# Kernel tuning notes

Hardware: AMD Instinct MI355X
Metric: run time of the kernel (lower is better)

Reference implementation:

```python
import jax, jax.numpy as jnp
import numpy as np

EMBED_DIM = 1024
NUM_HEADS = 16
NUM_KV_HEADS = 4
HEAD_DIM = 64
WINDOW_SIZE = 32
TOKENS_PER_FRAME = 64
BASE_T, BASE_D, BASE_B = 10000.0, 100.0, 100.0


def apply_3d_rope(x, pos_t, pos_d, pos_b):
    # x: (B, S, H, D); pos_*: (S,) int
    D = x.shape[-1]
    half = D // 2
    dim_idx = jnp.arange(half, dtype=jnp.float32)
    inv_freq = 1.0 / (BASE_T ** (2.0 * dim_idx / D))  # (half,)
    ang = (pos_t.astype(jnp.float32)[:, None] * inv_freq
           + pos_d.astype(jnp.float32)[:, None] * inv_freq * (BASE_T / BASE_D)
           + pos_b.astype(jnp.float32)[:, None] * inv_freq * (BASE_T / BASE_B))  # (S, half)
    cos = jnp.cos(ang)[None, :, None, :]
    sin = jnp.sin(ang)[None, :, None, :]
    x1 = x[..., 0::2]
    x2 = x[..., 1::2]
    y1 = x1 * cos - x2 * sin
    y2 = x1 * sin + x2 * cos
    return jnp.stack([y1, y2], axis=-1).reshape(x.shape)


def setup_inputs() -> dict:
    key = jax.random.key(0)
    ks = jax.random.split(key, 8)
    B, Sn, Lp = 1, 1024, 4096
    hidden_states = jax.random.normal(ks[0], (B, Sn, EMBED_DIM), dtype=jnp.float32)
    past_k = jax.random.normal(ks[1], (B, NUM_KV_HEADS, Lp, HEAD_DIM), dtype=jnp.float32)
    past_v = jax.random.normal(ks[2], (B, NUM_KV_HEADS, Lp, HEAD_DIM), dtype=jnp.float32)
    wq = jax.random.normal(ks[3], (EMBED_DIM, NUM_HEADS * HEAD_DIM), dtype=jnp.float32) * 0.02
    wk = jax.random.normal(ks[4], (EMBED_DIM, NUM_KV_HEADS * HEAD_DIM), dtype=jnp.float32) * 0.02
    wv = jax.random.normal(ks[5], (EMBED_DIM, NUM_KV_HEADS * HEAD_DIM), dtype=jnp.float32) * 0.02
    wo = jax.random.normal(ks[6], (NUM_HEADS * HEAD_DIM, EMBED_DIM), dtype=jnp.float32) * 0.02
    # frame-time positions: tokens_per_frame tokens share a frame time; past frames 0..63, new frames 64..79
    past_idx = jnp.arange(Lp, dtype=jnp.int32)
    new_idx = jnp.arange(Sn, dtype=jnp.int32)
    past_t = past_idx // TOKENS_PER_FRAME
    new_t = new_idx // TOKENS_PER_FRAME + Lp // TOKENS_PER_FRAME
    # 8x8 depth-by-bearing patch grid within each frame
    past_d = (past_idx % TOKENS_PER_FRAME) // 8
    past_b = past_idx % 8
    new_d = (new_idx % TOKENS_PER_FRAME) // 8
    new_b = new_idx % 8
    return dict(hidden_states=hidden_states, past_k=past_k, past_v=past_v,
                wq=wq, wk=wk, wv=wv, wo=wo,
                new_t=new_t, new_d=new_d, new_b=new_b,
                past_t=past_t, past_d=past_d, past_b=past_b)


def reference(hidden_states, past_k, past_v, wq, wk, wv, wo,
              new_t, new_d, new_b, past_t, past_d, past_b):
    B, Sn, _ = hidden_states.shape
    Lp = past_t.shape[0]
    Q = (hidden_states @ wq).reshape(B, Sn, NUM_HEADS, HEAD_DIM)
    Kn = (hidden_states @ wk).reshape(B, Sn, NUM_KV_HEADS, HEAD_DIM)
    Vn = (hidden_states @ wv).reshape(B, Sn, NUM_KV_HEADS, HEAD_DIM)
    Q = apply_3d_rope(Q, new_t, new_d, new_b)
    Kn = apply_3d_rope(Kn, new_t, new_d, new_b)
    Q = Q.transpose(0, 2, 1, 3)   # (B, H, Sn, D)
    Kn = Kn.transpose(0, 2, 1, 3)  # (B, KVH, Sn, D)
    Vn = Vn.transpose(0, 2, 1, 3)
    # Sliding-window truncation on frame time: torch does searchsorted + slice
    # (drop past keys with time < min_time). Masking those keys to -inf is
    # mathematically identical and jit-friendly (static shapes).
    min_time = new_t.max() - (WINDOW_SIZE - 1)
    past_keep = past_t >= min_time                                    # (Lp,)
    valid = jnp.concatenate([past_keep, jnp.ones((Sn,), dtype=bool)])  # (Lp+Sn,)
    pos_t = jnp.concatenate([past_t, new_t])
    K = jnp.concatenate([past_k, Kn], axis=2)  # (B, KVH, Lp+Sn, D)
    V = jnp.concatenate([past_v, Vn], axis=2)
    rep = NUM_HEADS // NUM_KV_HEADS
    K = jnp.repeat(K, rep, axis=1)  # (B, H, L, D) -- repeat_interleave semantics
    V = jnp.repeat(V, rep, axis=1)
    scores = jnp.einsum('bhqd,bhkd->bhqk', Q, K) / jnp.sqrt(jnp.float32(HEAD_DIM))
    mask = (pos_t[None, :] <= new_t[:, None]) & valid[None, :]  # (Sn, L) frame-causal + window
    scores = jnp.where(mask[None, None], scores, jnp.float32(-jnp.inf))
    attn = jax.nn.softmax(scores, axis=-1)
    attn = jnp.nan_to_num(attn)  # fully-masked rows -> 0 (matches torch nan_to_num)
    out = jnp.einsum('bhqk,bhkd->bhqd', attn, V)
    out = out.transpose(0, 2, 1, 3).reshape(B, Sn, NUM_HEADS * HEAD_DIM)
    out = out @ wo
    return out, Kn, Vn
```

## Files before the change

### kernel.cpp

```cpp
#include <hip/hip_runtime.h>
#include <math.h>

#define EMBED 1024
#define NH 16
#define NKV 4
#define HD 64
#define SN 1024
#define LP 4096
#define WIN 32

#define FREQ_C 0.4152410118609203f

typedef float floatx4 __attribute__((ext_vector_type(4)));
typedef __bf16 bf16x8 __attribute__((ext_vector_type(8)));

__global__ __launch_bounds__(256) void qkv_mfma_kernel(
    const float* __restrict__ hidden, const float* __restrict__ wq,
    const float* __restrict__ wk, const float* __restrict__ wv,
    const int* __restrict__ new_t, const int* __restrict__ new_d,
    const int* __restrict__ new_b,
    float* __restrict__ qws, float* __restrict__ knp, float* __restrict__ vnp)
{
    __shared__ __bf16 ASh[64][72];
    __shared__ __bf16 BSh[64][72];

    const int tid = threadIdx.x;
    const int lane = tid & 63, w = tid >> 6;
    const int g = lane >> 4, c = lane & 15;
    const int bx = blockIdx.x, by = blockIdx.y;

    int mode, ldb, cbase;
    const float* W;
    if (bx < 16)      { mode = 0; W = wq; ldb = 1024; cbase = bx * 64; }
    else if (bx < 20) { mode = 1; W = wk; ldb = 256;  cbase = (bx - 16) * 64; }
    else              { mode = 2; W = wv; ldb = 256;  cbase = (bx - 20) * 64; }

    const int arow = tid >> 2, ak = (tid & 3) * 16;
    const float* Ap = hidden + (size_t)(by * 64 + arow) * EMBED + ak;
    const int bn = tid & 63, bk0 = (tid >> 6) * 16;
    const float* Bp = W + (size_t)bk0 * ldb + cbase + bn;

    floatx4 acc[4] = {floatx4(0.f), floatx4(0.f), floatx4(0.f), floatx4(0.f)};

    float a0[16], b0[16];
#pragma unroll
    for (int i = 0; i < 4; i++)
        *(float4*)&a0[4 * i] = *(const float4*)(Ap + 4 * i);
#pragma unroll
    for (int j = 0; j < 16; j++) b0[j] = Bp[(size_t)j * ldb];

    const int strip = w * 16;

    for (int k0 = 0; k0 < EMBED; k0 += 64) {
        __syncthreads();
        {
            bf16x8 av0, av1, bv0, bv1;
#pragma unroll
            for (int j = 0; j < 8; j++) {
                av0[j] = (__bf16)a0[j];     av1[j] = (__bf16)a0[j + 8];
                bv0[j] = (__bf16)b0[j];     bv1[j] = (__bf16)b0[j + 8];
            }
            *(bf16x8*)&ASh[arow][ak] = av0;
            *(bf16x8*)&ASh[arow][ak + 8] = av1;
            *(bf16x8*)&BSh[bn][bk0] = bv0;
            *(bf16x8*)&BSh[bn][bk0 + 8] = bv1;
        }
        __syncthreads();
        if (k0 + 64 < EMBED) {
#pragma unroll
            for (int i = 0; i < 4; i++)
                *(float4*)&a0[4 * i] = *(const float4*)(Ap + k0 + 64 + 4 * i);
#pragma unroll
            for (int j = 0; j < 16; j++) b0[j] = Bp[(size_t)(k0 + 64 + j) * ldb];
        }
        bf16x8 af0 = *(const bf16x8*)&ASh[strip + c][g * 8];
        bf16x8 af1 = *(const bf16x8*)&ASh[strip + c][32 + g * 8];
#pragma unroll
        for (int t = 0; t < 4; t++) {
            bf16x8 bf0 = *(const bf16x8*)&BSh[t * 16 + c][g * 8];
            bf16x8 bf1 = *(const bf16x8*)&BSh[t * 16 + c][32 + g * 8];
            acc[t] = __builtin_amdgcn_mfma_f32_16x16x32_bf16(af0, bf0, acc[t], 0, 0, 0);
            acc[t] = __builtin_amdgcn_mfma_f32_16x16x32_bf16(af1, bf1, acc[t], 0, 0, 0);
        }
    }

    const int m0 = strip + g * 4;
    if (mode == 2) {
        const int kvh = bx - 20;
#pragma unroll
        for (int r = 0; r < 4; r++) {
            const int token = by * 64 + m0 + r;
#pragma unroll
            for (int t = 0; t < 4; t++)
                vnp[((size_t)kvh * SN + token) * HD + t * 16 + c] = acc[t][r];
        }
    } else {
        float fr[4];
#pragma unroll
        for (int t = 0; t < 4; t++) {
            const int d = (cbase + t * 16 + c) & 63;
            fr[t] = exp2f(-FREQ_C * (float)(d >> 1));
        }
        const int par = c & 1;
#pragma unroll
        for (int r = 0; r < 4; r++) {
            const int token = by * 64 + m0 + r;
            const float ft = (float)new_t[token];
            const float fdb = (float)(new_d[token] + new_b[token]);
#pragma unroll
            for (int t = 0; t < 4; t++) {
                const float ang = ft * fr[t] + fdb * (fr[t] * 100.0f);
                float sv, cv;
                sincosf(ang, &sv, &cv);
                const float x = acc[t][r];
                const float xp = __shfl_xor(x, 1, 64);
                const float y = par ? (xp * sv + x * cv) : (x * cv - xp * sv);
                if (mode == 0) {
                    qws[(size_t)token * EMBED + cbase + t * 16 + c] = y;
                } else {
                    const int kvh = bx - 16;
                    knp[((size_t)kvh * SN + token) * HD + t * 16 + c] = y;
                }
            }
        }
    }
}

__global__ __launch_bounds__(256) void out_mfma_kernel(
    const float* __restrict__ A, const float* __restrict__ W,
    float* __restrict__ C)
{
    __shared__ __bf16 ASh[64][72];
    __shared__ __bf16 BSh[64][72];

    const int tid = threadIdx.x;
    const int lane = tid & 63, w = tid >> 6;
    const int g = lane >> 4, c = lane & 15;
    const int bx = blockIdx.x, by = blockIdx.y;

    const int arow = tid >> 2, ak = (tid & 3) * 16;
    const float* Ap = A + (size_t)(by * 64 + arow) * EMBED + ak;
    const int bn = tid & 63, bk0 = (tid >> 6) * 16;
    const float* Bp = W + (size_t)bk0 * EMBED + bx * 64 + bn;

    floatx4 acc[4] = {floatx4(0.f), floatx4(0.f), floatx4(0.f), floatx4(0.f)};

    float a0[16], b0[16];
#pragma unroll
    for (int i = 0; i < 4; i++)
        *(float4*)&a0[4 * i] = *(const float4*)(Ap + 4 * i);
#pragma unroll
    for (int j = 0; j < 16; j++) b0[j] = Bp[(size_t)j * EMBED];

    const int strip = w * 16;

    for (int k0 = 0; k0 < EMBED; k0 += 64) {
        __syncthreads();
        {
            bf16x8 av0, av1, bv0, bv1;
#pragma unroll
            for (int j = 0; j < 8; j++) {
                av0[j] = (__bf16)a0[j];     av1[j] = (__bf16)a0[j + 8];
                bv0[j] = (__bf16)b0[j];     bv1[j] = (__bf16)b0[j + 8];
            }
            *(bf16x8*)&ASh[arow][ak] = av0;
            *(bf16x8*)&ASh[arow][ak + 8] = av1;
            *(bf16x8*)&BSh[bn][bk0] = bv0;
            *(bf16x8*)&BSh[bn][bk0 + 8] = bv1;
        }
        __syncthreads();
        if (k0 + 64 < EMBED) {
#pragma unroll
            for (int i = 0; i < 4; i++)
                *(float4*)&a0[4 * i] = *(const float4*)(Ap + k0 + 64 + 4 * i);
#pragma unroll
            for (int j = 0; j < 16; j++) b0[j] = Bp[(size_t)(k0 + 64 + j) * EMBED];
        }
        bf16x8 af0 = *(const bf16x8*)&ASh[strip + c][g * 8];
        bf16x8 af1 = *(const bf16x8*)&ASh[strip + c][32 + g * 8];
#pragma unroll
        for (int t = 0; t < 4; t++) {
            bf16x8 bf0 = *(const bf16x8*)&BSh[t * 16 + c][g * 8];
            bf16x8 bf1 = *(const bf16x8*)&BSh[t * 16 + c][32 + g * 8];
            acc[t] = __builtin_amdgcn_mfma_f32_16x16x32_bf16(af0, bf0, acc[t], 0, 0, 0);
            acc[t] = __builtin_amdgcn_mfma_f32_16x16x32_bf16(af1, bf1, acc[t], 0, 0, 0);
        }
    }

    const int m0 = strip + g * 4;
#pragma unroll
    for (int r = 0; r < 4; r++) {
        const int row = by * 64 + m0 + r;
#pragma unroll
        for (int t = 0; t < 4; t++)
            C[(size_t)row * EMBED + bx * 64 + t * 16 + c] = acc[t][r];
    }
}

#define PREFETCH_CHUNK(CI)                                                     \
    {                                                                          \
        const int base_ = (myStart + (CI)) << 6;                               \
        const int gk_ = base_ + skk;                                           \
        if (gk_ < Nk) {                                                        \
            const float* kp_ = (gk_ < nPast)                                   \
                ? past_k + ((size_t)(kvh * LP + p0 + gk_)) * HD + sd0          \
                : knp + ((size_t)(kvh * SN + (gk_ - nPast))) * HD + sd0;       \
            kb0 = *(const float4*)(kp_ + 0);                                   \
            kb1 = *(const float4*)(kp_ + 4);                                   \
            kb2 = *(const float4*)(kp_ + 8);                                   \
            kb3 = *(const float4*)(kp_ + 12);                                  \
        } else {                                                               \
            kb0 = kb1 = kb2 = kb3 = make_float4(0.f, 0.f, 0.f, 0.f);           \
        }                                                                      \
        const int gv0_ = base_ + 2 * kp2;                                      \
        if (gv0_ < Nk) {                                                       \
            const float* vp_ = (gv0_ < nPast)                                  \
                ? past_v + ((size_t)(kvh * LP + p0 + gv0_)) * HD + vdb         \
                : vnp + ((size_t)(kvh * SN + (gv0_ - nPast))) * HD + vdb;      \
            vb00 = *(const float4*)(vp_ + 0);                                  \
            vb01 = *(const float4*)(vp_ + 4);                                  \
        } else {                                                               \
            vb00 = vb01 = make_float4(0.f, 0.f, 0.f, 0.f);                     \
        }                                                                      \
        const int gv1_ = gv0_ + 1;                                             \
        if (gv1_ < Nk) {                                                       \
            const float* vp_ = (gv1_ < nPast)                                  \
                ? past_v + ((size_t)(kvh * LP + p0 + gv1_)) * HD + vdb         \
                : vnp + ((size_t)(kvh * SN + (gv1_ - nPast))) * HD + vdb;      \
            vb10 = *(const float4*)(vp_ + 0);                                  \
            vb11 = *(const float4*)(vp_ + 4);                                  \
        } else {                                                               \
            vb10 = vb11 = make_float4(0.f, 0.f, 0.f, 0.f);                     \
        }                                                                      \
        if (tid < 64) {                                                        \
            const int g2_ = base_ + tid;                                       \
            ptreg = (g2_ < Nk)                                                 \
                ? ((g2_ < nPast) ? past_t[p0 + g2_] : new_t[g2_ - nPast])      \
                : 0x7fffffff;                                                  \
        }                                                                      \
    }

__global__ __launch_bounds__(256) void attn_kernel(
    const float* __restrict__ qws, const float* __restrict__ past_k,
    const float* __restrict__ past_v, const float* __restrict__ knp,
    const float* __restrict__ vnp, const int* __restrict__ new_t,
    const int* __restrict__ past_t, float* __restrict__ opart,
    float* __restrict__ lpart)
{
    __shared__ __bf16 KS[64][72];
    __shared__ __bf16 VS[64][72];
    __shared__ __bf16 PS[64][72];
    __shared__ float MSK[64];

    const int tid = threadIdx.x;
    const int f = blockIdx.x, h = blockIdx.y, sidx = blockIdx.z;
    const int kvh = h >> 2;
    const int lane = tid & 63, w = tid >> 6;
    const int g = lane >> 4, c = lane & 15;

    const int tmax = new_t[SN - 1];
    const int min_time = tmax - (WIN - 1);
    const int qtf = new_t[f * 64];

    int lo = 0, hi = LP;
    while (lo < hi) {
        int mid = (lo + hi) >> 1;
        if (past_t[mid] >= min_time) hi = mid; else lo = mid + 1;
    }
    const int p0 = lo;
    const int nPast = LP - p0;
    const int Nk = nPast + (f + 1) * 64;

    const int nch = (Nk + 63) >> 6;
    const int qch = nch >> 2, rem = nch & 3;
    const int myCount = qch + (sidx < rem ? 1 : 0);
    const int myStart = sidx * qch + (sidx < rem ? sidx : rem);

    bf16x8 aQ[2];
    {
        const int q = f * 64 + w * 16 + c;
        const float* qp = qws + (size_t)q * EMBED + h * HD + g * 8;
#pragma unroll
        for (int s = 0; s < 2; s++) {
            float4 q0 = *(const float4*)(qp + s * 32);
            float4 q1 = *(const float4*)(qp + s * 32 + 4);
            bf16x8 a;
            a[0] = (__bf16)q0.x; a[1] = (__bf16)q0.y;
            a[2] = (__bf16)q0.z; a[3] = (__bf16)q0.w;
            a[4] = (__bf16)q1.x; a[5] = (__bf16)q1.y;
            a[6] = (__bf16)q1.z; a[7] = (__bf16)q1.w;
            aQ[s] = a;
        }
    }

    floatx4 oacc[4] = {floatx4(0.f), floatx4(0.f), floatx4(0.f), floatx4(0.f)};
    floatx4 lacc = floatx4(0.f);
    bf16x8 bOnes;
#pragma unroll
    for (int j = 0; j < 8; j++) bOnes[j] = (__bf16)1.0f;

    const float scale = 0.125f;

    const int skk = tid >> 2, sd0 = (tid & 3) * 16;
    const int kp2 = tid & 31, vdb = (tid >> 5) * 8;

    float4 kb0, kb1, kb2, kb3;
    float4 vb00, vb01, vb10, vb11;
    int ptreg = 0x7fffffff;

    if (myCount > 0) PREFETCH_CHUNK(0);

    for (int chi = 0; chi < myCount; ++chi) {
        __syncthreads();

        {
            bf16x8 t0, t1;
            t0[0] = (__bf16)kb0.x; t0[1] = (__bf16)kb0.y;
            t0[2] = (__bf16)kb0.z; t0[3] = (__bf16)kb0.w;
            t0[4] = (__bf16)kb1.x; t0[5] = (__bf16)kb1.y;
            t0[6] = (__bf16)kb1.z; t0[7] = (__bf16)kb1.w;
            t1[0] = (__bf16)kb2.x; t1[1] = (__bf16)kb2.y;
            t1[2] = (__bf16)kb2.z; t1[3] = (__bf16)kb2.w;
            t1[4] = (__bf16)kb3.x; t1[5] = (__bf16)kb3.y;
            t1[6] = (__bf16)kb3.z; t1[7] = (__bf16)kb3.w;
            *(bf16x8*)&KS[skk][sd0] = t0;
            *(bf16x8*)&KS[skk][sd0 + 8] = t1;
        }
        {
            float e0[8] = {vb00.x, vb00.y, vb00.z, vb00.w,
                           vb01.x, vb01.y, vb01.z, vb01.w};
            float e1[8] = {vb10.x, vb10.y, vb10.z, vb10.w,
                           vb11.x, vb11.y, vb11.z, vb11.w};
#pragma unroll
            for (int j = 0; j < 8; j++) {
                union { __bf16 b[2]; unsigned u; } pk;
                pk.b[0] = (__bf16)e0[j];
                pk.b[1] = (__bf16)e1[j];
                *(unsigned*)&VS[vdb + j][2 * kp2] = pk.u;
            }
        }
        if (tid < 64) {
            const int g2 = ((myStart + chi) << 6) + tid;
            const bool ok = (ptreg <= qtf) && ((g2 >= nPast) || (ptreg >= min_time));
            MSK[tid] = ok ? 0.f : -1e30f;
        }
        __syncthreads();

        if (chi + 1 < myCount) PREFETCH_CHUNK(chi + 1);

        floatx4 sacc[4];
#pragma unroll
        for (int t = 0; t < 4; t++) {
            sacc[t] = floatx4(0.f);
#pragma unroll
            for (int s = 0; s < 2; s++) {
                bf16x8 b = *(const bf16x8*)&KS[t * 16 + c][s * 32 + g * 8];
                sacc[t] = __builtin_amdgcn_mfma_f32_16x16x32_bf16(aQ[s], b, sacc[t], 0, 0, 0);
            }
        }

#pragma unroll
        for (int r = 0; r < 4; r++)
#pragma unroll
            for (int t = 0; t < 4; t++)
                PS[w * 16 + g * 4 + r][t * 16 + c] =
                    (__bf16)__expf(sacc[t][r] * scale + MSK[t * 16 + c]);

#pragma unroll
        for (int s = 0; s < 2; s++) {
            bf16x8 a = *(const bf16x8*)&PS[w * 16 + c][s * 32 + g * 8];
            lacc = __builtin_amdgcn_mfma_f32_16x16x32_bf16(a, bOnes, lacc, 0, 0, 0);
#pragma unroll
            for (int t = 0; t < 4; t++) {
                bf16x8 b = *(const bf16x8*)&VS[t * 16 + c][s * 32 + g * 8];
                oacc[t] = __builtin_amdgcn_mfma_f32_16x16x32_bf16(a, b, oacc[t], 0, 0, 0);
            }
        }
    }

    float* Op = opart + ((size_t)(f * 16 + h) * 4 + sidx) * 4096;
    float* lp = lpart + ((size_t)(f * 16 + h) * 4 + sidx) * 64;
#pragma unroll
    for (int r = 0; r < 4; r++) {
        const int q = w * 16 + g * 4 + r;
#pragma unroll
        for (int t = 0; t < 4; t++)
            Op[(size_t)q * 64 + t * 16 + c] = oacc[t][r];
        if (c == 0) lp[q] = lacc[r];
    }
}

__global__ __launch_bounds__(256) void attn_merge_kernel(
    const float* __restrict__ opart, const float* __restrict__ lpart,
    float* __restrict__ ctx)
{
    const int f = blockIdx.x, h = blockIdx.y;
    const int tid = threadIdx.x;
    const int q = tid >> 2, d0 = (tid & 3) * 16;
    const size_t fh = (size_t)(f * 16 + h);

    float l = 0.f;
#pragma unroll
    for (int s = 0; s < 4; s++) l += lpart[(fh * 4 + s) * 64 + q];
    const float inv = (l > 0.f) ? (1.f / l) : 0.f;

    float o[16] = {};
#pragma unroll
    for (int s = 0; s < 4; s++) {
        const float* Os = opart + (fh * 4 + s) * 4096 + (size_t)q * 64 + d0;
#pragma unroll
        for (int v = 0; v < 4; v++) {
            float4 ov = *(const float4*)(Os + v * 4);
            o[v * 4 + 0] += ov.x;
            o[v * 4 + 1] += ov.y;
            o[v * 4 + 2] += ov.z;
            o[v * 4 + 3] += ov.w;
        }
    }
    float* cp = ctx + (size_t)(f * 64 + q) * EMBED + h * HD + d0;
#pragma unroll
    for (int v = 0; v < 4; v++)
        *(float4*)(cp + v * 4) = make_float4(o[v * 4] * inv, o[v * 4 + 1] * inv,
                                             o[v * 4 + 2] * inv, o[v * 4 + 3] * inv);
}

extern "C" void kernel_launch(void* const* d_in, const int* in_sizes, int n_in,
                              void* d_out, int out_size, void* d_ws, size_t ws_size,
                              hipStream_t stream) {
    const float* hidden = (const float*)d_in[0];
    const float* past_k = (const float*)d_in[1];
    const float* past_v = (const float*)d_in[2];
    const float* wq     = (const float*)d_in[3];
    const float* wk     = (const float*)d_in[4];
    const float* wv     = (const float*)d_in[5];
    const float* wo     = (const float*)d_in[6];
    const int* new_t    = (const int*)d_in[7];
    const int* new_d    = (const int*)d_in[8];
    const int* new_b    = (const int*)d_in[9];
    const int* past_t   = (const int*)d_in[10];

    float* out = (float*)d_out;
    float* knp = out + SN * EMBED;
    float* vnp = knp + NKV * SN * HD;

    float* qws   = (float*)d_ws;
    float* lpart = qws + (size_t)SN * EMBED;
    float* opart = lpart + (size_t)16 * 16 * 4 * 64;
    float* ctx   = opart + (size_t)16 * 16 * 4 * 4096;

    qkv_mfma_kernel<<<dim3(24, 16), 256, 0, stream>>>(
        hidden, wq, wk, wv, new_t, new_d, new_b, qws, knp, vnp);
    attn_kernel<<<dim3(16, 16, 4), 256, 0, stream>>>(
        qws, past_k, past_v, knp, vnp, new_t, past_t, opart, lpart);
    attn_merge_kernel<<<dim3(16, 16), 256, 0, stream>>>(opart, lpart, ctx);
    out_mfma_kernel<<<dim3(16, 16), 256, 0, stream>>>(ctx, wo, out);
}
```

Baseline: 156.8 us.

## Pre-convert inputs and weights to transposed bf16 and remap attention grid per XCD

Adds a prep kernel that converts hidden states to bf16 and transposes and converts wq/wk/wv/wo to bf16 so the GEMM kernels load contiguous 16-byte bf16 vectors instead of strided fp32 scalars. The merge kernel writes its context in bf16 to halve traffic into the output projection. The attention grid is flattened and remapped so blocks sharing a KV head are dispatched to the same XCD, aiming for better L2 reuse of past K/V. In exchange it adds an extra launch and re-converts the weights on every call.

```diff
diff --git a/kernel.cpp b/kernel.cpp
--- a/kernel.cpp
+++ b/kernel.cpp
@@ -14,9 +14,71 @@
 typedef float floatx4 __attribute__((ext_vector_type(4)));
 typedef __bf16 bf16x8 __attribute__((ext_vector_type(8)));
 
-__global__ __launch_bounds__(256) void qkv_mfma_kernel(
+__global__ __launch_bounds__(256) void prep_kernel(
     const float* __restrict__ hidden, const float* __restrict__ wq,
     const float* __restrict__ wk, const float* __restrict__ wv,
+    const float* __restrict__ wo,
+    __bf16* __restrict__ hidb, __bf16* __restrict__ wqT,
+    __bf16* __restrict__ wkT, __bf16* __restrict__ wvT,
+    __bf16* __restrict__ woT)
+{
+    const int jb = blockIdx.x, tid = threadIdx.x;
+    if (jb >= 640) {
+        const size_t base = (size_t)(jb - 640) * 4096 + (size_t)tid * 16;
+        float4 f0 = *(const float4*)(hidden + base);
+        float4 f1 = *(const float4*)(hidden + base + 4);
+        float4 f2 = *(const float4*)(hidden + base + 8);
+        float4 f3 = *(const float4*)(hidden + base + 12);
+        bf16x8 o0, o1;
+        o0[0] = (__bf16)f0.x; o0[1] = (__bf16)f0.y;
+        o0[2] = (__bf16)f0.z; o0[3] = (__bf16)f0.w;
+        o0[4] = (__bf16)f1.x; o0[5] = (__bf16)f1.y;
+        o0[6] = (__bf16)f1.z; o0[7] = (__bf16)f1.w;
+        o1[0] = (__bf16)f2.x; o1[1] = (__bf16)f2.y;
+        o1[2] = (__bf16)f2.z; o1[3] = (__bf16)f2.w;
+        o1[4] = (__bf16)f3.x; o1[5] = (__bf16)f3.y;
+        o1[6] = (__bf16)f3.z; o1[7] = (__bf16)f3.w;
+        *(bf16x8*)(hidb + base) = o0;
+        *(bf16x8*)(hidb + base + 8) = o1;
+        return;
+    }
+    const float* src; __bf16* dst; int N, tk, tn;
+    if (jb < 256)      { src = wq; dst = wqT; N = 1024; tk = jb >> 4;         tn = jb & 15; }
+    else if (jb < 320) { src = wk; dst = wkT; N = 256;  tk = (jb - 256) >> 2; tn = (jb - 256) & 3; }
+    else if (jb < 384) { src = wv; dst = wvT; N = 256;  tk = (jb - 320) >> 2; tn = (jb - 320) & 3; }
+    else               { src = wo; dst = woT; N = 1024; tk = (jb - 384) >> 4; tn = (jb - 384) & 15; }
+
+    __shared__ float T[64][65];
+    {
+        const int r = tid >> 2, c0 = (tid & 3) * 16;
+        const float* sp = src + (size_t)(tk * 64 + r) * N + tn * 64 + c0;
+        float4 v0 = *(const float4*)(sp + 0);
+        float4 v1 = *(const float4*)(sp + 4);
+        float4 v2 = *(const float4*)(sp + 8);
+        float4 v3 = *(const float4*)(sp + 12);
+        *(float4*)&T[r][c0 + 0] = v0;
+        *(float4*)&T[r][c0 + 4] = v1;
+        *(float4*)&T[r][c0 + 8] = v2;
+        *(float4*)&T[r][c0 + 12] = v3;
+    }
+    __syncthreads();
+    {
+        const int n = tid >> 2, k0 = (tid & 3) * 16;
+        bf16x8 o0, o1;
+#pragma unroll
+        for (int j = 0; j < 8; j++) {
+            o0[j] = (__bf16)T[k0 + j][n];
+            o1[j] = (__bf16)T[k0 + 8 + j][n];
+        }
+        __bf16* dp = dst + (size_t)(tn * 64 + n) * 1024 + tk * 64 + k0;
+        *(bf16x8*)dp = o0;
+        *(bf16x8*)(dp + 8) = o1;
+    }
+}
+
+__global__ __launch_bounds__(256) void qkv_mfma_kernel(
+    const __bf16* __restrict__ hidb, const __bf16* __restrict__ wqT,
+    const __bf16* __restrict__ wkT, const __bf16* __restrict__ wvT,
     const int* __restrict__ new_t, const int* __restrict__ new_d,
     const int* __restrict__ new_b,
     float* __restrict__ qws, float* __restrict__ knp, float* __restrict__ vnp)
@@ -29,49 +91,38 @@
     const int g = lane >> 4, c = lane & 15;
     const int bx = blockIdx.x, by = blockIdx.y;
 
-    int mode, ldb, cbase;
-    const float* W;
-    if (bx < 16)      { mode = 0; W = wq; ldb = 1024; cbase = bx * 64; }
-    else if (bx < 20) { mode = 1; W = wk; ldb = 256;  cbase = (bx - 16) * 64; }
-    else              { mode = 2; W = wv; ldb = 256;  cbase = (bx - 20) * 64; }
+    int mode, cbase;
+    const __bf16* W;
+    if (bx < 16)      { mode = 0; W = wqT; cbase = bx * 64; }
+    else if (bx < 20) { mode = 1; W = wkT; cbase = (bx - 16) * 64; }
+    else              { mode = 2; W = wvT; cbase = (bx - 20) * 64; }
 
     const int arow = tid >> 2, ak = (tid & 3) * 16;
-    const float* Ap = hidden + (size_t)(by * 64 + arow) * EMBED + ak;
+    const __bf16* Ap = hidb + (size_t)(by * 64 + arow) * EMBED + ak;
     const int bn = tid & 63, bk0 = (tid >> 6) * 16;
-    const float* Bp = W + (size_t)bk0 * ldb + cbase + bn;
+    const __bf16* Bp = W + (size_t)(cbase + bn) * 1024 + bk0;
 
     floatx4 acc[4] = {floatx4(0.f), floatx4(0.f), floatx4(0.f), floatx4(0.f)};
 
-    float a0[16], b0[16];
-#pragma unroll
-    for (int i = 0; i < 4; i++)
-        *(float4*)&a0[4 * i] = *(const float4*)(Ap + 4 * i);
-#pragma unroll
-    for (int j = 0; j < 16; j++) b0[j] = Bp[(size_t)j * ldb];
+    bf16x8 a0 = *(const bf16x8*)(Ap);
+    bf16x8 a1 = *(const bf16x8*)(Ap + 8);
+    bf16x8 b0 = *(const bf16x8*)(Bp);
+    bf16x8 b1 = *(const bf16x8*)(Bp + 8);
 
     const int strip = w * 16;
 
     for (int k0 = 0; k0 < EMBED; k0 += 64) {
         __syncthreads();
-        {
-            bf16x8 av0, av1, bv0, bv1;
-#pragma unroll
-            for (int j = 0; j < 8; j++) {
-                av0[j] = (__bf16)a0[j];     av1[j] = (__bf16)a0[j + 8];
-                bv0[j] = (__bf16)b0[j];     bv1[j] = (__bf16)b0[j + 8];
-            }
-            *(bf16x8*)&ASh[arow][ak] = av0;
-            *(bf16x8*)&ASh[arow][ak + 8] = av1;
-            *(bf16x8*)&BSh[bn][bk0] = bv0;
-            *(bf16x8*)&BSh[bn][bk0 + 8] = bv1;
-        }
+        *(bf16x8*)&ASh[arow][ak] = a0;
+        *(bf16x8*)&ASh[arow][ak + 8] = a1;
+        *(bf16x8*)&BSh[bn][bk0] = b0;
+        *(bf16x8*)&BSh[bn][bk0 + 8] = b1;
         __syncthreads();
         if (k0 + 64 < EMBED) {
-#pragma unroll
-            for (int i = 0; i < 4; i++)
-                *(float4*)&a0[4 * i] = *(const float4*)(Ap + k0 + 64 + 4 * i);
-#pragma unroll
-            for (int j = 0; j < 16; j++) b0[j] = Bp[(size_t)(k0 + 64 + j) * ldb];
+            a0 = *(const bf16x8*)(Ap + k0 + 64);
+            a1 = *(const bf16x8*)(Ap + k0 + 72);
+            b0 = *(const bf16x8*)(Bp + k0 + 64);
+            b1 = *(const bf16x8*)(Bp + k0 + 72);
         }
         bf16x8 af0 = *(const bf16x8*)&ASh[strip + c][g * 8];
         bf16x8 af1 = *(const bf16x8*)&ASh[strip + c][32 + g * 8];
@@ -127,7 +178,7 @@
 }
 
 __global__ __launch_bounds__(256) void out_mfma_kernel(
-    const float* __restrict__ A, const float* __restrict__ W,
+    const __bf16* __restrict__ ctxb, const __bf16* __restrict__ woT,
     float* __restrict__ C)
 {
     __shared__ __bf16 ASh[64][72];
@@ -139,42 +190,31 @@
     const int bx = blockIdx.x, by = blockIdx.y;
 
     const int arow = tid >> 2, ak = (tid & 3) * 16;
-    const float* Ap = A + (size_t)(by * 64 + arow) * EMBED + ak;
+    const __bf16* Ap = ctxb + (size_t)(by * 64 + arow) * EMBED + ak;
     const int bn = tid & 63, bk0 = (tid >> 6) * 16;
-    const float* Bp = W + (size_t)bk0 * EMBED + bx * 64 + bn;
+    const __bf16* Bp = woT + (size_t)(bx * 64 + bn) * 1024 + bk0;
 
     floatx4 acc[4] = {floatx4(0.f), floatx4(0.f), floatx4(0.f), floatx4(0.f)};
 
-    float a0[16], b0[16];
-#pragma unroll
-    for (int i = 0; i < 4; i++)
-        *(float4*)&a0[4 * i] = *(const float4*)(Ap + 4 * i);
-#pragma unroll
-    for (int j = 0; j < 16; j++) b0[j] = Bp[(size_t)j * EMBED];
+    bf16x8 a0 = *(const bf16x8*)(Ap);
+    bf16x8 a1 = *(const bf16x8*)(Ap + 8);
+    bf16x8 b0 = *(const bf16x8*)(Bp);
+    bf16x8 b1 = *(const bf16x8*)(Bp + 8);
 
     const int strip = w * 16;
 
     for (int k0 = 0; k0 < EMBED; k0 += 64) {
         __syncthreads();
-        {
-            bf16x8 av0, av1, bv0, bv1;
-#pragma unroll
-            for (int j = 0; j < 8; j++) {
-                av0[j] = (__bf16)a0[j];     av1[j] = (__bf16)a0[j + 8];
-                bv0[j] = (__bf16)b0[j];     bv1[j] = (__bf16)b0[j + 8];
-            }
-            *(bf16x8*)&ASh[arow][ak] = av0;
-            *(bf16x8*)&ASh[arow][ak + 8] = av1;
-            *(bf16x8*)&BSh[bn][bk0] = bv0;
-            *(bf16x8*)&BSh[bn][bk0 + 8] = bv1;
-        }
+        *(bf16x8*)&ASh[arow][ak] = a0;
+        *(bf16x8*)&ASh[arow][ak + 8] = a1;
+        *(bf16x8*)&BSh[bn][bk0] = b0;
+        *(bf16x8*)&BSh[bn][bk0 + 8] = b1;
         __syncthreads();
         if (k0 + 64 < EMBED) {
-#pragma unroll
-            for (int i = 0; i < 4; i++)
-                *(float4*)&a0[4 * i] = *(const float4*)(Ap + k0 + 64 + 4 * i);
-#pragma unroll
-            for (int j = 0; j < 16; j++) b0[j] = Bp[(size_t)(k0 + 64 + j) * EMBED];
+            a0 = *(const bf16x8*)(Ap + k0 + 64);
+            a1 = *(const bf16x8*)(Ap + k0 + 72);
+            b0 = *(const bf16x8*)(Bp + k0 + 64);
+            b1 = *(const bf16x8*)(Bp + k0 + 72);
         }
         bf16x8 af0 = *(const bf16x8*)&ASh[strip + c][g * 8];
         bf16x8 af1 = *(const bf16x8*)&ASh[strip + c][32 + g * 8];
@@ -253,8 +293,15 @@
     __shared__ float MSK[64];
 
     const int tid = threadIdx.x;
-    const int f = blockIdx.x, h = blockIdx.y, sidx = blockIdx.z;
-    const int kvh = h >> 2;
+    const int i = blockIdx.x;
+    const int xcd = i & 7;
+    const int kvh = xcd >> 1;
+    const int jj = i >> 3;
+    const int hloc = jj & 3;
+    const int f = (jj >> 2) & 15;
+    const int sidx = (xcd & 1) | (((jj >> 6) & 1) << 1);
+    const int h = kvh * 4 + hloc;
+
     const int lane = tid & 63, w = tid >> 6;
     const int g = lane >> 4, c = lane & 15;
 
@@ -392,7 +439,7 @@
 
 __global__ __launch_bounds__(256) void attn_merge_kernel(
     const float* __restrict__ opart, const float* __restrict__ lpart,
-    float* __restrict__ ctx)
+    __bf16* __restrict__ ctxb)
 {
     const int f = blockIdx.x, h = blockIdx.y;
     const int tid = threadIdx.x;
@@ -417,11 +464,15 @@
             o[v * 4 + 3] += ov.w;
         }
     }
-    float* cp = ctx + (size_t)(f * 64 + q) * EMBED + h * HD + d0;
-#pragma unroll
-    for (int v = 0; v < 4; v++)
-        *(float4*)(cp + v * 4) = make_float4(o[v * 4] * inv, o[v * 4 + 1] * inv,
-                                             o[v * 4 + 2] * inv, o[v * 4 + 3] * inv);
+    bf16x8 o0, o1;
+#pragma unroll
+    for (int j = 0; j < 8; j++) {
+        o0[j] = (__bf16)(o[j] * inv);
+        o1[j] = (__bf16)(o[8 + j] * inv);
+    }
+    __bf16* cp = ctxb + (size_t)(f * 64 + q) * EMBED + h * HD + d0;
+    *(bf16x8*)cp = o0;
+    *(bf16x8*)(cp + 8) = o1;
 }
 
 extern "C" void kernel_launch(void* const* d_in, const int* in_sizes, int n_in,
@@ -446,12 +497,19 @@
     float* qws   = (float*)d_ws;
     float* lpart = qws + (size_t)SN * EMBED;
     float* opart = lpart + (size_t)16 * 16 * 4 * 64;
-    float* ctx   = opart + (size_t)16 * 16 * 4 * 4096;
-
+    __bf16* hidb = (__bf16*)(opart + (size_t)16 * 16 * 4 * 4096);
+    __bf16* wqT  = hidb + (size_t)SN * EMBED;
+    __bf16* wkT  = wqT + (size_t)1024 * 1024;
+    __bf16* wvT  = wkT + (size_t)256 * 1024;
+    __bf16* woT  = wvT + (size_t)256 * 1024;
+    __bf16* ctxb = woT + (size_t)1024 * 1024;
+
+    prep_kernel<<<dim3(896), 256, 0, stream>>>(
+        hidden, wq, wk, wv, wo, hidb, wqT, wkT, wvT, woT);
     qkv_mfma_kernel<<<dim3(24, 16), 256, 0, stream>>>(
-        hidden, wq, wk, wv, new_t, new_d, new_b, qws, knp, vnp);
-    attn_kernel<<<dim3(16, 16, 4), 256, 0, stream>>>(
+        hidb, wqT, wkT, wvT, new_t, new_d, new_b, qws, knp, vnp);
+    attn_kernel<<<dim3(1024), 256, 0, stream>>>(
         qws, past_k, past_v, knp, vnp, new_t, past_t, opart, lpart);
-    attn_merge_kernel<<<dim3(16, 16), 256, 0, stream>>>(opart, lpart, ctx);
-    out_mfma_kernel<<<dim3(16, 16), 256, 0, stream>>>(ctx, wo, out);
+    attn_merge_kernel<<<dim3(16, 16), 256, 0, stream>>>(opart, lpart, ctxb);
+    out_mfma_kernel<<<dim3(16, 16), 256, 0, stream>>>(ctxb, woT, out);
 }
```

Result: no change. 155.1 us (-1.1%).
